# Kernel tuning notes

Hardware: AMD Instinct MI355X
Metric: run time of the kernel (lower is better)

The kernel has to match this reference:

```python
import jax, jax.numpy as jnp
import numpy as np

N, C, H, W = 2, 32, 128, 256
MAX_DISP = 48


def setup_inputs() -> dict:
    key = jax.random.key(0)
    k1, k2 = jax.random.split(key)
    l_fmap = jax.random.normal(k1, (N, C, H, W), dtype=jnp.float32)
    r_fmap = jax.random.normal(k2, (N, C, H, W), dtype=jnp.float32)
    return {"l_fmap": l_fmap, "r_fmap": r_fmap}


def reference(l_fmap, r_fmap):
    # Faithful to make_cost_volume_naive: cost[:, :, d, :, d:] = l[..., d:] - r[..., :-d],
    # positions w < d keep the init value 1.0. Fully vectorized over disparity.
    n, c, h, w = l_fmap.shape
    d_idx = jnp.arange(MAX_DISP)[:, None]          # [D,1]
    w_idx = jnp.arange(w)[None, :]                 # [1,W]
    src = jnp.clip(w_idx - d_idx, 0, w - 1)        # [D,W] gather index into r's width
    # r shifted right by d per disparity: [N,C,H,D,W] -> [N,C,D,H,W]
    r_shift = jnp.moveaxis(r_fmap[:, :, :, src], 3, 2)
    mask = (w_idx >= d_idx)[None, None, :, None, :]  # [1,1,D,1,W]
    cost = jnp.where(mask, l_fmap[:, :, None, :, :] - r_shift, jnp.float32(1.0))
    return cost  # [N,C,D,H,W]
```

## Files before the change

kernel.cpp:

```cpp
#include <hip/hip_runtime.h>

constexpr int N = 2, C = 32, H = 128, W = 256, MAX_DISP = 48;
constexpr int W4 = W / 4;
constexpr int TOTAL4 = N * C * MAX_DISP * H * W4;

__global__ __launch_bounds__(256) void cost_volume_kernel(
    const float* __restrict__ l,
    const float* __restrict__ r,
    float4* __restrict__ out)
{
    int idx = blockIdx.x * blockDim.x + threadIdx.x;
    if (idx >= TOTAL4) return;

    int w4 = idx & (W4 - 1);
    int t  = idx >> 6;
    int h  = t & (H - 1);
    t >>= 7;
    int d  = t % MAX_DISP;
    int nc = t / MAX_DISP;

    int w0 = w4 << 2;
    const float* lrow = l + ((size_t)nc * H + h) * W;
    const float* rrow = r + ((size_t)nc * H + h) * W;

    float4 lv = *reinterpret_cast<const float4*>(lrow + w0);

    float4 o;
    o.x = (w0 + 0 >= d) ? lv.x - rrow[w0 + 0 - d] : 1.0f;
    o.y = (w0 + 1 >= d) ? lv.y - rrow[w0 + 1 - d] : 1.0f;
    o.z = (w0 + 2 >= d) ? lv.z - rrow[w0 + 2 - d] : 1.0f;
    o.w = (w0 + 3 >= d) ? lv.w - rrow[w0 + 3 - d] : 1.0f;

    out[idx] = o;
}

extern "C" void kernel_launch(void* const* d_in, const int* in_sizes, int n_in,
                              void* d_out, int out_size, void* d_ws, size_t ws_size,
                              hipStream_t stream)
{
    const float* l = (const float*)d_in[0];
    const float* r = (const float*)d_in[1];
    float4* out = (float4*)d_out;

    constexpr int BLOCK = 256;
    constexpr int GRID = (TOTAL4 + BLOCK - 1) / BLOCK;
    cost_volume_kernel<<<GRID, BLOCK, 0, stream>>>(l, r, out);
}
```

Before: 490.9 us.

## Reuse each (n,c,h) row across all disparities via LDS staging

Each block now handles one (n,c,h) row. It loads the r row into shared memory with a zero pad and keeps the l float4 in registers, then loops over all 48 disparities, with four waves splitting them. This removes redundant global reads of l and r for every disparity and removes the per-thread index decode. The cost is fewer, longer-lived blocks, strided stores across disparity planes, and possible unaligned LDS reads.

```diff
diff --git a/kernel.cpp b/kernel.cpp
--- a/kernel.cpp
+++ b/kernel.cpp
@@ -1,37 +1,50 @@
 #include <hip/hip_runtime.h>
 
-constexpr int N = 2, C = 32, H = 128, W = 256, MAX_DISP = 48;
+constexpr int N = 2, C = 32, H = 128, W = 256, D = 48;
+constexpr int NC = N * C;
 constexpr int W4 = W / 4;
-constexpr int TOTAL4 = N * C * MAX_DISP * H * W4;
+constexpr int PASSES = D / 4;
 
 __global__ __launch_bounds__(256) void cost_volume_kernel(
     const float* __restrict__ l,
     const float* __restrict__ r,
     float4* __restrict__ out)
 {
-    int idx = blockIdx.x * blockDim.x + threadIdx.x;
-    if (idx >= TOTAL4) return;
+    __shared__ float r_lds[D + W];
 
-    int w4 = idx & (W4 - 1);
-    int t  = idx >> 6;
-    int h  = t & (H - 1);
-    t >>= 7;
-    int d  = t % MAX_DISP;
-    int nc = t / MAX_DISP;
+    const int blk = blockIdx.x;
+    const int h   = blk & (H - 1);
+    const int nc  = blk >> 7;
 
-    int w0 = w4 << 2;
-    const float* lrow = l + ((size_t)nc * H + h) * W;
-    const float* rrow = r + ((size_t)nc * H + h) * W;
+    const float* lrow = l + (size_t)blk * W;
+    const float* rrow = r + (size_t)blk * W;
 
-    float4 lv = *reinterpret_cast<const float4*>(lrow + w0);
+    const int t = threadIdx.x;
+    r_lds[D + t] = rrow[t];
+    if (t < D) r_lds[t] = 0.0f;
 
-    float4 o;
-    o.x = (w0 + 0 >= d) ? lv.x - rrow[w0 + 0 - d] : 1.0f;
-    o.y = (w0 + 1 >= d) ? lv.y - rrow[w0 + 1 - d] : 1.0f;
-    o.z = (w0 + 2 >= d) ? lv.z - rrow[w0 + 2 - d] : 1.0f;
-    o.w = (w0 + 3 >= d) ? lv.w - rrow[w0 + 3 - d] : 1.0f;
+    const int lane = t & 63;
+    const int wv   = t >> 6;
+    const int w0   = lane << 2;
 
-    out[idx] = o;
+    const float4 lv = *reinterpret_cast<const float4*>(lrow + w0);
+
+    __syncthreads();
+
+    float4* obase = out + (((size_t)nc * D * H) + h) * W4 + lane;
+    const size_t dstride = (size_t)H * W4;
+
+    #pragma unroll
+    for (int pass = 0; pass < PASSES; ++pass) {
+        const int d = wv + pass * 4;
+        const float* rs = r_lds + (D - d) + w0;
+        float4 o;
+        o.x = (w0 + 0 >= d) ? lv.x - rs[0] : 1.0f;
+        o.y = (w0 + 1 >= d) ? lv.y - rs[1] : 1.0f;
+        o.z = (w0 + 2 >= d) ? lv.z - rs[2] : 1.0f;
+        o.w = (w0 + 3 >= d) ? lv.w - rs[3] : 1.0f;
+        obase[(size_t)d * dstride] = o;
+    }
 }
 
 extern "C" void kernel_launch(void* const* d_in, const int* in_sizes, int n_in,
@@ -42,7 +55,6 @@
     const float* r = (const float*)d_in[1];
     float4* out = (float4*)d_out;
 
-    constexpr int BLOCK = 256;
-    constexpr int GRID = (TOTAL4 + BLOCK - 1) / BLOCK;
-    cost_volume_kernel<<<GRID, BLOCK, 0, stream>>>(l, r, out);
+    constexpr int GRID = NC * H;
+    cost_volume_kernel<<<GRID, 256, 0, stream>>>(l, r, out);
 }
```

Measured after the change: 405.2 us. 1.21x faster.
